# Kernel tuning notes

Hardware: AMD Instinct MI355X
Metric: run time of the kernel (lower is better)

Reference implementation:

```python
import jax, jax.numpy as jnp
import numpy as np

B, D, OUT = 256, 63, 128
DP = D + 1  # 64


def setup_inputs() -> dict:
    key = jax.random.key(0)
    k1, k2, k3, k4, k5 = jax.random.split(key, 5)
    return {
        "x": jax.random.normal(k1, (B, D), dtype=jnp.float32),
        "protein_output": jax.random.normal(k2, (B, D), dtype=jnp.float32),
        "dynamic_output": jax.random.normal(k3, (B, D), dtype=jnp.float32),
        "W": jax.random.normal(k4, (DP ** 3, OUT), dtype=jnp.float32) * 0.02,
        "b": jax.random.normal(k5, (OUT,), dtype=jnp.float32) * 0.02,
    }


def reference(x, protein_output, dynamic_output, W, b):
    bsz = x.shape[0]
    ones = jnp.ones((bsz, 1), dtype=x.dtype)
    a = jnp.concatenate([x, ones], axis=1)               # [B, D+1]
    p = jnp.concatenate([protein_output, ones], axis=1)   # [B, D+1]
    d = jnp.concatenate([dynamic_output, ones], axis=1)   # [B, D+1]
    # rank-1 trilinear outer product, flattened row-major: idx = (i*(D+1)+j)*(D+1)+k
    ab = jnp.einsum('bi,bj->bij', a, p)                   # [B, D+1, D+1]
    abc = jnp.einsum('bij,bk->bijk', ab, d)               # [B, D+1, D+1, D+1]
    feat = abc.reshape(bsz, -1)                           # [B, (D+1)^3]
    return feat @ W + b                                   # [B, OUT]
```

## Files before the change

kernel.cpp:

```cpp
#include <hip/hip_runtime.h>
#include <hip/hip_bf16.h>

typedef __attribute__((ext_vector_type(8))) short short8v;
typedef __attribute__((ext_vector_type(4))) float floatx4;

__device__ __forceinline__ unsigned int pkbf(float a, float b) {
  __hip_bfloat162 h = __float22bfloat162_rn(make_float2(a, b));
  union { __hip_bfloat162 h; unsigned int u; } c; c.h = h;
  return c.u;
}

__global__ void bias_init(const float* __restrict__ bias, float* __restrict__ out) {
  int idx = blockIdx.x * 256 + threadIdx.x;
  out[idx] = bias[idx & 127];
}

__global__ __launch_bounds__(128)
void reduce_k(const float* __restrict__ part, const float* __restrict__ bias,
              float* __restrict__ out) {
  int o = blockIdx.x * 128 + threadIdx.x;
  const float* p = part + o;
  float s0 = 0.f, s1 = 0.f, s2 = 0.f, s3 = 0.f;
  #pragma unroll 8
  for (int c = 0; c < 256; c += 4) {
    s0 += p[(long)c * 32768];
    s1 += p[(long)(c + 1) * 32768];
    s2 += p[(long)(c + 2) * 32768];
    s3 += p[(long)(c + 3) * 32768];
  }
  out[o] = s0 + s1 + s2 + s3 + bias[o & 127];
}

__global__ __launch_bounds__(512, 2)
void tfn_gemm(const float* __restrict__ X, const float* __restrict__ P,
              const float* __restrict__ Dyn, const float* __restrict__ W,
              float* __restrict__ part, float* __restrict__ out, int use_ws) {
  __shared__ float p_lds[16][256];

  const int tid = threadIdx.x;
  const int wv = tid >> 6, lane = tid & 63;
  const int q = lane >> 4, l16 = lane & 15;
  const int r = wv & 3;
  const int cg = wv >> 2;

  const int c = blockIdx.x;
  const int i = c >> 2;
  const int j0 = (c & 3) << 4;
  const long gk0 = (long)c << 10;

  for (int idx = tid; idx < 256 * 16; idx += 512) {
    int bb = idx >> 4, jj = idx & 15;
    int j = j0 + jj;
    p_lds[jj][bb] = (j < 63) ? P[bb * 63 + j] : 1.0f;
  }

  float e[4][2][8];
  #pragma unroll
  for (int rt = 0; rt < 4; ++rt) {
    int brow = (r << 6) + (rt << 4) + l16;
    float av = (i < 63) ? X[brow * 63 + i] : 1.0f;
    #pragma unroll
    for (int h = 0; h < 2; ++h) {
      int kb = (h << 5) + (q << 3);
      #pragma unroll
      for (int t = 0; t < 8; ++t) {
        int k = kb + t;
        float dv = (k < 63) ? Dyn[brow * 63 + k] : 1.0f;
        e[rt][h][t] = av * dv;
      }
    }
  }

  floatx4 acc[4][4];
  #pragma unroll
  for (int a = 0; a < 4; ++a)
    #pragma unroll
    for (int b = 0; b < 4; ++b) acc[a][b] = (floatx4)0.0f;

  __syncthreads();

  const float* wstep = W + (gk0 + (q << 3)) * 128 + (cg << 6) + l16;

  float wA[4][8], wB[4][8];

  #pragma unroll
  for (int nt = 0; nt < 4; ++nt)
    #pragma unroll
    for (int t = 0; t < 8; ++t)
      wA[nt][t] = wstep[t * 128 + nt * 16];

  for (int jj = 0; jj < 16; ++jj) {
    float pb[4];
    #pragma unroll
    for (int rt = 0; rt < 4; ++rt)
      pb[rt] = p_lds[jj][(r << 6) + (rt << 4) + l16];

    {
      const float* wp = wstep + ((long)(2 * jj + 1) << 12);
      #pragma unroll
      for (int nt = 0; nt < 4; ++nt)
        #pragma unroll
        for (int t = 0; t < 8; ++t)
          wB[nt][t] = wp[t * 128 + nt * 16];

      union { short8v v; unsigned int u[4]; } fb[4], fa[4];
      #pragma unroll
      for (int nt = 0; nt < 4; ++nt)
        #pragma unroll
        for (int v2 = 0; v2 < 4; ++v2)
          fb[nt].u[v2] = pkbf(wA[nt][2 * v2], wA[nt][2 * v2 + 1]);
      #pragma unroll
      for (int rt = 0; rt < 4; ++rt)
        #pragma unroll
        for (int v2 = 0; v2 < 4; ++v2)
          fa[rt].u[v2] = pkbf(pb[rt] * e[rt][0][2 * v2], pb[rt] * e[rt][0][2 * v2 + 1]);
      #pragma unroll
      for (int rt = 0; rt < 4; ++rt)
        #pragma unroll
        for (int nt = 0; nt < 4; ++nt)
          acc[rt][nt] = __builtin_amdgcn_mfma_f32_16x16x32_bf16(
              fa[rt].v, fb[nt].v, acc[rt][nt], 0, 0, 0);
    }

    {
      if (jj < 15) {
        const float* wp = wstep + ((long)(2 * jj + 2) << 12);
        #pragma unroll
        for (int nt = 0; nt < 4; ++nt)
          #pragma unroll
          for (int t = 0; t < 8; ++t)
            wA[nt][t] = wp[t * 128 + nt * 16];
      }

      union { short8v v; unsigned int u[4]; } fb[4], fa[4];
      #pragma unroll
      for (int nt = 0; nt < 4; ++nt)
        #pragma unroll
        for (int v2 = 0; v2 < 4; ++v2)
          fb[nt].u[v2] = pkbf(wB[nt][2 * v2], wB[nt][2 * v2 + 1]);
      #pragma unroll
      for (int rt = 0; rt < 4; ++rt)
        #pragma unroll
        for (int v2 = 0; v2 < 4; ++v2)
          fa[rt].u[v2] = pkbf(pb[rt] * e[rt][1][2 * v2], pb[rt] * e[rt][1][2 * v2 + 1]);
      #pragma unroll
      for (int rt = 0; rt < 4; ++rt)
        #pragma unroll
        for (int nt = 0; nt < 4; ++nt)
          acc[rt][nt] = __builtin_amdgcn_mfma_f32_16x16x32_bf16(
              fa[rt].v, fb[nt].v, acc[rt][nt], 0, 0, 0);
    }
  }

  if (use_ws) {
    float* pt = part + ((long)c << 15);
    #pragma unroll
    for (int rt = 0; rt < 4; ++rt)
      #pragma unroll
      for (int nt = 0; nt < 4; ++nt) {
        int col = (cg << 6) + (nt << 4) + l16;
        #pragma unroll
        for (int g = 0; g < 4; ++g) {
          int brow = (r << 6) + (rt << 4) + (q << 2) + g;
          pt[brow * 128 + col] = acc[rt][nt][g];
        }
      }
  } else {
    #pragma unroll
    for (int rt = 0; rt < 4; ++rt)
      #pragma unroll
      for (int nt = 0; nt < 4; ++nt) {
        int col = (cg << 6) + (nt << 4) + l16;
        #pragma unroll
        for (int g = 0; g < 4; ++g) {
          int brow = (r << 6) + (rt << 4) + (q << 2) + g;
          atomicAdd(&out[brow * 128 + col], acc[rt][nt][g]);
        }
      }
  }
}

extern "C" void kernel_launch(void* const* d_in, const int* in_sizes, int n_in,
                              void* d_out, int out_size, void* d_ws, size_t ws_size,
                              hipStream_t stream) {
  const float* x   = (const float*)d_in[0];
  const float* p   = (const float*)d_in[1];
  const float* dyn = (const float*)d_in[2];
  const float* W   = (const float*)d_in[3];
  const float* b   = (const float*)d_in[4];
  float* out = (float*)d_out;

  const size_t need = (size_t)256 * 32768 * sizeof(float);
  if (d_ws != nullptr && ws_size >= need) {
    float* part = (float*)d_ws;
    tfn_gemm<<<256, 512, 0, stream>>>(x, p, dyn, W, part, out, 1);
    reduce_k<<<256, 128, 0, stream>>>(part, b, out);
  } else {
    bias_init<<<128, 256, 0, stream>>>(b, out);
    tfn_gemm<<<256, 512, 0, stream>>>(x, p, dyn, W, nullptr, out, 0);
  }
}
```

Before: 240.6 us.

## Pre-transpose W to bf16 K-contiguous layout and load vectorized B fragments

A new kernel converts W to bf16 and transposes it so each output column's K values are contiguous. The GEMM can then load MFMA B fragments as 16-byte vectors and skip the fp32-to-bf16 packing in its inner loop. The cost is an extra full pass over W on every call (a 128MB fp32 read plus a 64MB bf16 write) and more workspace. The GEMM's inner loop is restructured into double-buffered fragment loads; the atomic fallback path is kept as a separate kernel.

```diff
diff --git a/kernel.cpp b/kernel.cpp
--- a/kernel.cpp
+++ b/kernel.cpp
@@ -3,6 +3,9 @@
 
 typedef __attribute__((ext_vector_type(8))) short short8v;
 typedef __attribute__((ext_vector_type(4))) float floatx4;
+
+#define KTOT 262144L
+#define WT_BYTES (128L * KTOT * 2L)
 
 __device__ __forceinline__ unsigned int pkbf(float a, float b) {
   __hip_bfloat162 h = __float22bfloat162_rn(make_float2(a, b));
@@ -10,9 +13,33 @@
   return c.u;
 }
 
-__global__ void bias_init(const float* __restrict__ bias, float* __restrict__ out) {
-  int idx = blockIdx.x * 256 + threadIdx.x;
-  out[idx] = bias[idx & 127];
+__global__ __launch_bounds__(512)
+void transpose_w(const float* __restrict__ W, short* __restrict__ Wt) {
+  __shared__ float T[128][129];
+  const long k0 = (long)blockIdx.x << 7;
+  const int tid = threadIdx.x;
+
+  {
+    const int n = tid & 127, ks = tid >> 7;
+    #pragma unroll 8
+    for (int r = 0; r < 32; ++r) {
+      int k = (ks << 5) + r;
+      T[k][n] = W[(k0 + k) * 128 + n];
+    }
+  }
+  __syncthreads();
+  {
+    const int n = tid >> 2, kq = tid & 3;
+    #pragma unroll
+    for (int u = 0; u < 4; ++u) {
+      int kb = (kq << 5) + (u << 3);
+      union { short8v v; unsigned int w[4]; } pk;
+      #pragma unroll
+      for (int v2 = 0; v2 < 4; ++v2)
+        pk.w[v2] = pkbf(T[kb + 2 * v2][n], T[kb + 2 * v2 + 1][n]);
+      *(short8v*)(Wt + (long)n * KTOT + k0 + kb) = pk.v;
+    }
+  }
 }
 
 __global__ __launch_bounds__(128)
@@ -32,9 +59,9 @@
 }
 
 __global__ __launch_bounds__(512, 2)
-void tfn_gemm(const float* __restrict__ X, const float* __restrict__ P,
-              const float* __restrict__ Dyn, const float* __restrict__ W,
-              float* __restrict__ part, float* __restrict__ out, int use_ws) {
+void tfn_gemm_bt(const float* __restrict__ X, const float* __restrict__ P,
+                 const float* __restrict__ Dyn, const short* __restrict__ Wt,
+                 float* __restrict__ part) {
   __shared__ float p_lds[16][256];
 
   const int tid = threadIdx.x;
@@ -79,41 +106,134 @@
 
   __syncthreads();
 
+  const short* wrow = Wt + ((long)((cg << 6) + l16)) * KTOT + gk0 + (q << 3);
+  const short* wp[4];
+  #pragma unroll
+  for (int nt = 0; nt < 4; ++nt) wp[nt] = wrow + (long)nt * (KTOT << 4);
+
+#define COMPUTE(jj, buf)                                                          \
+  {                                                                               \
+    float pb[4];                                                                  \
+    _Pragma("unroll") for (int rt = 0; rt < 4; ++rt)                              \
+        pb[rt] = p_lds[jj][(r << 6) + (rt << 4) + l16];                           \
+    _Pragma("unroll") for (int h = 0; h < 2; ++h) {                               \
+      union { short8v v; unsigned int u[4]; } fa[4];                              \
+      _Pragma("unroll") for (int rt = 0; rt < 4; ++rt)                            \
+          _Pragma("unroll") for (int v2 = 0; v2 < 4; ++v2)                        \
+              fa[rt].u[v2] = pkbf(pb[rt] * e[rt][h][2 * v2],                      \
+                                  pb[rt] * e[rt][h][2 * v2 + 1]);                 \
+      _Pragma("unroll") for (int rt = 0; rt < 4; ++rt)                            \
+          _Pragma("unroll") for (int nt = 0; nt < 4; ++nt)                        \
+              acc[rt][nt] = __builtin_amdgcn_mfma_f32_16x16x32_bf16(              \
+                  fa[rt].v, (buf)[h][nt], acc[rt][nt], 0, 0, 0);                  \
+    }                                                                             \
+  }
+
+  short8v bufA[2][4], bufB[2][4];
+  #pragma unroll
+  for (int h = 0; h < 2; ++h)
+    #pragma unroll
+    for (int nt = 0; nt < 4; ++nt)
+      bufA[h][nt] = *(const short8v*)(wp[nt] + h * 32);
+
+  for (int jj2 = 0; jj2 < 8; ++jj2) {
+    const int jjA = jj2 << 1, jjB = jjA + 1;
+    #pragma unroll
+    for (int h = 0; h < 2; ++h)
+      #pragma unroll
+      for (int nt = 0; nt < 4; ++nt)
+        bufB[h][nt] = *(const short8v*)(wp[nt] + ((jjB << 1) + h) * 32);
+    COMPUTE(jjA, bufA);
+    #pragma unroll
+    for (int h = 0; h < 2; ++h)
+      #pragma unroll
+      for (int nt = 0; nt < 4; ++nt)
+        bufA[h][nt] = *(const short8v*)(wp[nt] + (((jjB + 1) << 1) + h) * 32);
+    COMPUTE(jjB, bufB);
+  }
+#undef COMPUTE
+
+  float* pt = part + ((long)c << 15);
+  #pragma unroll
+  for (int rt = 0; rt < 4; ++rt)
+    #pragma unroll
+    for (int nt = 0; nt < 4; ++nt) {
+      int col = (cg << 6) + (nt << 4) + l16;
+      #pragma unroll
+      for (int g = 0; g < 4; ++g) {
+        int brow = (r << 6) + (rt << 4) + (q << 2) + g;
+        pt[brow * 128 + col] = acc[rt][nt][g];
+      }
+    }
+}
+
+__global__ void bias_init(const float* __restrict__ bias, float* __restrict__ out) {
+  int idx = blockIdx.x * 256 + threadIdx.x;
+  out[idx] = bias[idx & 127];
+}
+
+__global__ __launch_bounds__(512, 2)
+void tfn_gemm_fb(const float* __restrict__ X, const float* __restrict__ P,
+                 const float* __restrict__ Dyn, const float* __restrict__ W,
+                 float* __restrict__ out) {
+  __shared__ float p_lds[16][256];
+  const int tid = threadIdx.x;
+  const int wv = tid >> 6, lane = tid & 63;
+  const int q = lane >> 4, l16 = lane & 15;
+  const int r = wv & 3, cg = wv >> 2;
+  const int c = blockIdx.x;
+  const int i = c >> 2;
+  const int j0 = (c & 3) << 4;
+  const long gk0 = (long)c << 10;
+
+  for (int idx = tid; idx < 256 * 16; idx += 512) {
+    int bb = idx >> 4, jj = idx & 15;
+    int j = j0 + jj;
+    p_lds[jj][bb] = (j < 63) ? P[bb * 63 + j] : 1.0f;
+  }
+  float e[4][2][8];
+  #pragma unroll
+  for (int rt = 0; rt < 4; ++rt) {
+    int brow = (r << 6) + (rt << 4) + l16;
+    float av = (i < 63) ? X[brow * 63 + i] : 1.0f;
+    #pragma unroll
+    for (int h = 0; h < 2; ++h)
+      #pragma unroll
+      for (int t = 0; t < 8; ++t) {
+        int k = (h << 5) + (q << 3) + t;
+        e[rt][h][t] = av * ((k < 63) ? Dyn[brow * 63 + k] : 1.0f);
+      }
+  }
+  floatx4 acc[4][4];
+  #pragma unroll
+  for (int a = 0; a < 4; ++a)
+    #pragma unroll
+    for (int b = 0; b < 4; ++b) acc[a][b] = (floatx4)0.0f;
+  __syncthreads();
+
   const float* wstep = W + (gk0 + (q << 3)) * 128 + (cg << 6) + l16;
-
-  float wA[4][8], wB[4][8];
-
-  #pragma unroll
-  for (int nt = 0; nt < 4; ++nt)
-    #pragma unroll
-    for (int t = 0; t < 8; ++t)
-      wA[nt][t] = wstep[t * 128 + nt * 16];
-
   for (int jj = 0; jj < 16; ++jj) {
     float pb[4];
     #pragma unroll
-    for (int rt = 0; rt < 4; ++rt)
-      pb[rt] = p_lds[jj][(r << 6) + (rt << 4) + l16];
-
-    {
-      const float* wp = wstep + ((long)(2 * jj + 1) << 12);
-      #pragma unroll
-      for (int nt = 0; nt < 4; ++nt)
-        #pragma unroll
-        for (int t = 0; t < 8; ++t)
-          wB[nt][t] = wp[t * 128 + nt * 16];
-
+    for (int rt = 0; rt < 4; ++rt) pb[rt] = p_lds[jj][(r << 6) + (rt << 4) + l16];
+    #pragma unroll
+    for (int h = 0; h < 2; ++h) {
+      const int s = (jj << 1) | h;
       union { short8v v; unsigned int u[4]; } fb[4], fa[4];
       #pragma unroll
-      for (int nt = 0; nt < 4; ++nt)
+      for (int nt = 0; nt < 4; ++nt) {
+        const float* wpq = wstep + ((long)s << 12) + nt * 16;
+        float wv8[8];
+        #pragma unroll
+        for (int t = 0; t < 8; ++t) wv8[t] = wpq[t * 128];
+        #pragma unroll
+        for (int v2 = 0; v2 < 4; ++v2) fb[nt].u[v2] = pkbf(wv8[2 * v2], wv8[2 * v2 + 1]);
+      }
+      #pragma unroll
+      for (int rt = 0; rt < 4; ++rt)
         #pragma unroll
         for (int v2 = 0; v2 < 4; ++v2)
-          fb[nt].u[v2] = pkbf(wA[nt][2 * v2], wA[nt][2 * v2 + 1]);
-      #pragma unroll
-      for (int rt = 0; rt < 4; ++rt)
-        #pragma unroll
-        for (int v2 = 0; v2 < 4; ++v2)
-          fa[rt].u[v2] = pkbf(pb[rt] * e[rt][0][2 * v2], pb[rt] * e[rt][0][2 * v2 + 1]);
+          fa[rt].u[v2] = pkbf(pb[rt] * e[rt][h][2 * v2], pb[rt] * e[rt][h][2 * v2 + 1]);
       #pragma unroll
       for (int rt = 0; rt < 4; ++rt)
         #pragma unroll
@@ -121,63 +241,18 @@
           acc[rt][nt] = __builtin_amdgcn_mfma_f32_16x16x32_bf16(
               fa[rt].v, fb[nt].v, acc[rt][nt], 0, 0, 0);
     }
-
-    {
-      if (jj < 15) {
-        const float* wp = wstep + ((long)(2 * jj + 2) << 12);
-        #pragma unroll
-        for (int nt = 0; nt < 4; ++nt)
-          #pragma unroll
-          for (int t = 0; t < 8; ++t)
-            wA[nt][t] = wp[t * 128 + nt * 16];
-      }
-
-      union { short8v v; unsigned int u[4]; } fb[4], fa[4];
-      #pragma unroll
-      for (int nt = 0; nt < 4; ++nt)
-        #pragma unroll
-        for (int v2 = 0; v2 < 4; ++v2)
-          fb[nt].u[v2] = pkbf(wB[nt][2 * v2], wB[nt][2 * v2 + 1]);
-      #pragma unroll
-      for (int rt = 0; rt < 4; ++rt)
-        #pragma unroll
-        for (int v2 = 0; v2 < 4; ++v2)
-          fa[rt].u[v2] = pkbf(pb[rt] * e[rt][1][2 * v2], pb[rt] * e[rt][1][2 * v2 + 1]);
-      #pragma unroll
-      for (int rt = 0; rt < 4; ++rt)
-        #pragma unroll
-        for (int nt = 0; nt < 4; ++nt)
-          acc[rt][nt] = __builtin_amdgcn_mfma_f32_16x16x32_bf16(
-              fa[rt].v, fb[nt].v, acc[rt][nt], 0, 0, 0);
-    }
-  }
-
-  if (use_ws) {
-    float* pt = part + ((long)c << 15);
-    #pragma unroll
-    for (int rt = 0; rt < 4; ++rt)
-      #pragma unroll
-      for (int nt = 0; nt < 4; ++nt) {
-        int col = (cg << 6) + (nt << 4) + l16;
-        #pragma unroll
-        for (int g = 0; g < 4; ++g) {
-          int brow = (r << 6) + (rt << 4) + (q << 2) + g;
-          pt[brow * 128 + col] = acc[rt][nt][g];
-        }
-      }
-  } else {
-    #pragma unroll
-    for (int rt = 0; rt < 4; ++rt)
-      #pragma unroll
-      for (int nt = 0; nt < 4; ++nt) {
-        int col = (cg << 6) + (nt << 4) + l16;
-        #pragma unroll
-        for (int g = 0; g < 4; ++g) {
-          int brow = (r << 6) + (rt << 4) + (q << 2) + g;
-          atomicAdd(&out[brow * 128 + col], acc[rt][nt][g]);
-        }
-      }
-  }
+  }
+  #pragma unroll
+  for (int rt = 0; rt < 4; ++rt)
+    #pragma unroll
+    for (int nt = 0; nt < 4; ++nt) {
+      int col = (cg << 6) + (nt << 4) + l16;
+      #pragma unroll
+      for (int g = 0; g < 4; ++g) {
+        int brow = (r << 6) + (rt << 4) + (q << 2) + g;
+        atomicAdd(&out[brow * 128 + col], acc[rt][nt][g]);
+      }
+    }
 }
 
 extern "C" void kernel_launch(void* const* d_in, const int* in_sizes, int n_in,
@@ -190,13 +265,15 @@
   const float* b   = (const float*)d_in[4];
   float* out = (float*)d_out;
 
-  const size_t need = (size_t)256 * 32768 * sizeof(float);
+  const size_t need = (size_t)WT_BYTES + (size_t)256 * 32768 * sizeof(float);
   if (d_ws != nullptr && ws_size >= need) {
-    float* part = (float*)d_ws;
-    tfn_gemm<<<256, 512, 0, stream>>>(x, p, dyn, W, part, out, 1);
+    short* Wt   = (short*)d_ws;
+    float* part = (float*)((char*)d_ws + WT_BYTES);
+    transpose_w<<<2048, 512, 0, stream>>>(W, Wt);
+    tfn_gemm_bt<<<256, 512, 0, stream>>>(x, p, dyn, Wt, part);
     reduce_k<<<256, 128, 0, stream>>>(part, b, out);
   } else {
     bias_init<<<128, 256, 0, stream>>>(b, out);
-    tfn_gemm<<<256, 512, 0, stream>>>(x, p, dyn, W, nullptr, out, 0);
-  }
-}
+    tfn_gemm_fb<<<256, 512, 0, stream>>>(x, p, dyn, W, out);
+  }
+}
```

Measured after the change: 288.6 us. +20.0%, slower.
